# Optimization experiments

Measured on AMD Instinct MI355X. Metric: run time of the kernel, lower is better.

## Reference

```python
import jax, jax.numpy as jnp
import numpy as np

R = 8            # LoRA rank (cfg.EXPERT_LOW_RANK)
E = 4            # expert count for proj (cfg.EXPERT_NUM)
TOPK_PCT = 50    # cfg.topk_tempalte == cfg.topk_search == 50, percent mode


def linear_experts(x, W, b, routeW, A, Bm, scaling):
    # LinearExperts.forward: frozen linear + softmax-routed sum of LoRA experts.
    res = x @ W.T + b
    rw = jax.nn.softmax((x @ routeW.T).astype(jnp.float32), axis=-1).astype(res.dtype)  # [B,N,E]
    z = jnp.einsum('bnc,erc->bner', x, A)      # [B,N,E,r]
    d = jnp.einsum('bner,ecr->bnec', z, Bm)    # [B,N,E,C_out]
    return res + jnp.einsum('bne,bnec->bnc', rw, d) * scaling


def merged_qkv(x, W, b, A, Bm, scaling):
    # loralib MergedLinear, enable_lora=[True,True,True]: grouped LoRA over q/k/v blocks.
    base = x @ W.T + b                          # [B,N,3C]
    z = jnp.einsum('bnc,grc->bngr', x, A)       # [B,N,3,r]
    d = jnp.einsum('bngr,gcr->bngc', z, Bm)     # [B,N,3,C]
    Bsz, N = x.shape[0], x.shape[1]
    return base + d.reshape(Bsz, N, -1) * scaling


def softmax_w_top(attn, top):
    # topk -> exp(v - v_max) -> normalize -> scatter back into zeros (rest exactly 0)
    vals, idx = jax.lax.top_k(attn, top)        # vals sorted desc, vals[...,0] is max
    ex = jnp.exp(vals - vals[..., :1])
    ex = ex / jnp.sum(ex, axis=-1, keepdims=True)
    Bh, Hh, Mh, _ = attn.shape
    bi = jnp.arange(Bh)[:, None, None, None]
    hi = jnp.arange(Hh)[None, :, None, None]
    mi = jnp.arange(Mh)[None, None, :, None]
    return jnp.zeros_like(attn).at[bi, hi, mi, idx].set(ex.astype(attn.dtype))


def setup_inputs() -> dict:
    key = jax.random.key(0)
    ks = jax.random.split(key, 32)
    B, N_m, N_s, C, H = 2, 576, 1024, 768, 12
    N = N_m + N_s
    hd = C // H
    N_mem = 1600
    s = 0.02
    inp = {
        'x': jax.random.normal(ks[0], (B, N, C), jnp.float32),
        'id_total': jax.random.normal(ks[1], (B, N_m, C), jnp.float32),
        'mem_k': jax.random.normal(ks[2], (B, H, N_mem, hd), jnp.float32),
        'mem_v': jax.random.normal(ks[3], (B, H, N_mem, hd), jnp.float32),
        # qkv MergedLinear
        'W_qkv': jax.random.normal(ks[4], (3 * C, C), jnp.float32) * s,
        'b_qkv': jnp.zeros((3 * C,), jnp.float32),
        'A_qkv': jax.random.normal(ks[5], (3, R, C), jnp.float32) * s,
        'B_qkv': jax.random.normal(ks[6], (3, C, R), jnp.float32) * s,
        # proj LinearExperts (lora_num=E)
        'W_proj': jax.random.normal(ks[7], (C, C), jnp.float32) * s,
        'b_proj': jnp.zeros((C,), jnp.float32),
        'routeW_proj': jax.random.normal(ks[8], (E, C), jnp.float32) * s,
        'A_proj': jax.random.normal(ks[9], (E, R, C), jnp.float32) * s,
        'B_proj': jax.random.normal(ks[10], (E, C, R), jnp.float32) * s,
        # linear_ID_K LinearExperts (lora_num=1, out=num_heads)
        'W_idk': jax.random.normal(ks[11], (H, C), jnp.float32) * s,
        'b_idk': jnp.zeros((H,), jnp.float32),
        'routeW_idk': jax.random.normal(ks[12], (1, C), jnp.float32) * s,
        'A_idk': jax.random.normal(ks[13], (1, R, C), jnp.float32) * s,
        'B_idk': jax.random.normal(ks[14], (1, H, R), jnp.float32) * s,
        # linear_ID_V LinearExperts (lora_num=1, out=dim)
        'W_idv': jax.random.normal(ks[15], (C, C), jnp.float32) * s,
        'b_idv': jnp.zeros((C,), jnp.float32),
        'routeW_idv': jax.random.normal(ks[16], (1, C), jnp.float32) * s,
        'A_idv': jax.random.normal(ks[17], (1, R, C), jnp.float32) * s,
        'B_idv': jax.random.normal(ks[18], (1, C, R), jnp.float32) * s,
        'id_add': 1,
    }
    return inp


def reference(x, id_total, mem_k, mem_v,
              W_qkv, b_qkv, A_qkv, B_qkv,
              W_proj, b_proj, routeW_proj, A_proj, B_proj,
              W_idk, b_idk, routeW_idk, A_idk, B_idk,
              W_idv, b_idv, routeW_idv, A_idv, B_idv,
              id_add):
    B, N, C = x.shape
    H = 12
    hd = C // H
    N_m = id_total.shape[1]
    N_s = N - N_m
    scale = hd ** -0.5
    scaling = 1.0 / R  # lora_alpha=1 default

    qkv = merged_qkv(x, W_qkv, b_qkv, A_qkv, B_qkv, scaling)          # [B,N,3C]
    qkv = qkv.reshape(B, N, 3, H, hd).transpose(2, 0, 3, 1, 4)        # [3,B,H,N,hd]
    q, k, v = qkv[0], qkv[1], qkv[2]
    k_m, k_s = k[:, :, :N_m], k[:, :, N_m:]
    v_m, v_s = v[:, :, :N_m], v[:, :, N_m:]

    # key_value_id: ID gating fused into memory K/V (id_add=True path)
    ID_K = linear_experts(id_total, W_idk, b_idk, routeW_idk, A_idk, B_idk, scaling)  # [B,N_m,H]
    ID_V = linear_experts(id_total, W_idv, b_idv, routeW_idv, A_idv, B_idv, scaling)  # [B,N_m,C]
    k_m = k_m * (1.0 + jnp.tanh(ID_K)).transpose(0, 2, 1)[..., None]                  # [B,H,N_m,hd]
    v_m_flat = v_m.transpose(0, 2, 1, 3).reshape(B, N_m, C) + ID_V                    # [B,N_m,C]
    v_m = v_m_flat.reshape(B, N_m, H, hd).transpose(0, 2, 1, 3)                       # [B,H,N_m,hd]
    v_add_id = jnp.concatenate([v_m, v_s], axis=2)                                    # [B,H,N,hd]

    q = q * scale
    q_m, q_s = q[:, :, :N_m], q[:, :, N_m:]

    # memory-token attention with top-k softmax (percent mode)
    attn_m = jnp.einsum('bhmd,bhnd->bhmn', q_m, k_m)
    top_m = TOPK_PCT * N_m // 100
    attn_m = softmax_w_top(attn_m, top_m)
    x_m = jnp.einsum('bhmn,bhnd->bhmd', attn_m, v_m).transpose(0, 2, 1, 3).reshape(B, N_m, C)

    # search-token attention over [cached memory, all current tokens]
    k_full = jnp.concatenate([mem_k, k], axis=2)
    v_full = jnp.concatenate([mem_v, v_add_id], axis=2)
    L = k_full.shape[2]
    attn_s = jnp.einsum('bhsd,bhld->bhsl', q_s, k_full)
    top_s = TOPK_PCT * L // 100
    attn_s = softmax_w_top(attn_s, top_s)
    x_s = jnp.einsum('bhsl,bhld->bhsd', attn_s, v_full).transpose(0, 2, 1, 3).reshape(B, N_s, C)

    out = jnp.concatenate([x_m, x_s], axis=1)
    out = linear_experts(out, W_proj, b_proj, routeW_proj, A_proj, B_proj, scaling)
    return (out, k_m, v_m)
```

## Files before the change

kernel.cpp:

```cpp
#include <hip/hip_runtime.h>
#include <hip/hip_bf16.h>

#define BN 2
#define NH 12
#define NTOK 1600
#define NM 576
#define NS 1024
#define CD 768
#define HD 64

typedef unsigned short u16;
typedef unsigned int u32;
typedef __attribute__((ext_vector_type(8))) short short8;
typedef __attribute__((ext_vector_type(4))) float f32x4;

__device__ __forceinline__ float fbits(u32 u) { return __uint_as_float(u); }
__device__ __forceinline__ u16 f2b(float f) {
    u32 u = __float_as_uint(f);
    u32 r = u + 0x7FFFu + ((u >> 16) & 1u);
    return (u16)(r >> 16);
}
__device__ __forceinline__ float b2f(u16 s) { return fbits(((u32)s) << 16); }
__device__ __forceinline__ u32 flip16(u32 u) {
    return (u & 0x8000u) ? (0xFFFFu & ~u) : (u | 0x8000u);
}
__device__ __forceinline__ float key2f(u32 k) {
    u32 b = (k & 0x8000u) ? (k & 0x7FFFu) : (0xFFFFu & ~k);
    return fbits(b << 16);
}
__device__ __forceinline__ float wave_red(float p) {
#pragma unroll
    for (int off = 1; off < 64; off <<= 1) p += __shfl_xor(p, off);
    return p;
}

__device__ __forceinline__ float dot768_ff(const float* __restrict__ a,
                                           const float* __restrict__ b) {
    float s = 0.f;
    for (int c = 0; c < CD; c += 4) {
        float4 fa = *(const float4*)(a + c);
        float4 fb = *(const float4*)(b + c);
        s += fa.x * fb.x + fa.y * fb.y + fa.z * fb.z + fa.w * fb.w;
    }
    return s;
}

__global__ __launch_bounds__(256) void small_dots(const float* __restrict__ x,
                                                  const float* __restrict__ Aq,
                                                  float* __restrict__ zq,
                                                  const float* __restrict__ id,
                                                  const float* __restrict__ Aik,
                                                  const float* __restrict__ Aiv,
                                                  const float* __restrict__ Wik,
                                                  const float* __restrict__ bik,
                                                  const float* __restrict__ Bik,
                                                  float* __restrict__ ziv,
                                                  float* __restrict__ IDK) {
    __shared__ float dres[28];
    const int blk = blockIdx.x;
    const int tid = threadIdx.x, lane = tid & 63, wv = tid >> 6;
    if (blk < 3200) {
        const float* xr = x + (size_t)blk * CD;
#pragma unroll
        for (int t = 0; t < 6; ++t) {
            const int q = wv * 6 + t;
            const float* ar = Aq + (size_t)q * CD;
            float p = 0.f;
#pragma unroll
            for (int c = 0; c < 12; ++c) p += xr[lane + c * 64] * ar[lane + c * 64];
            p = wave_red(p);
            if (lane == 0) zq[(size_t)blk * 24 + q] = p;
        }
    } else {
        const int m = blk - 3200;
        const float* xr = id + (size_t)m * CD;
#pragma unroll
        for (int t = 0; t < 7; ++t) {
            const int q = wv * 7 + t;
            const float* ar = (q < 8) ? Aik + (size_t)q * CD
                            : (q < 16) ? Aiv + (size_t)(q - 8) * CD
                                       : Wik + (size_t)(q - 16) * CD;
            float p = 0.f;
#pragma unroll
            for (int c = 0; c < 12; ++c) p += xr[lane + c * 64] * ar[lane + c * 64];
            p = wave_red(p);
            if (lane == 0) dres[q] = p;
        }
        __syncthreads();
        if (tid < 8) ziv[(size_t)m * 8 + tid] = dres[8 + tid];
        if (tid < 12) {
            float v = dres[16 + tid] + bik[tid];
            float lo = 0.f;
#pragma unroll
            for (int r = 0; r < 8; ++r) lo += dres[r] * Bik[tid * 8 + r];
            IDK[m * NH + tid] = v + 0.125f * lo;
        }
    }
}

__global__ __launch_bounds__(256) void stage_all(const float* __restrict__ x,
                                                 const float* __restrict__ zq,
                                                 u16* __restrict__ x_aug,
                                                 const float* __restrict__ Wq,
                                                 const float* __restrict__ Bq,
                                                 u16* __restrict__ wqkv_aug,
                                                 const float* __restrict__ Wp,
                                                 const float* __restrict__ Bp,
                                                 u16* __restrict__ wproj_aug,
                                                 const float* __restrict__ mk,
                                                 u16* __restrict__ kseq,
                                                 const float* __restrict__ mv,
                                                 u16* __restrict__ vt,
                                                 const float* __restrict__ id,
                                                 const float* __restrict__ ziv,
                                                 u16* __restrict__ id_aug,
                                                 const float* __restrict__ Widv,
                                                 const float* __restrict__ Bidv,
                                                 u16* __restrict__ widv_aug) {
    __shared__ float tile[64][65];
    const int blk = blockIdx.x;
    const int tid = threadIdx.x;
    if (blk < 1250) {
        const int idx = blk * 256 + tid;
        const int m = idx / 100, c8 = idx - m * 100;
        short8 v;
        if (c8 < 96) {
            const float* s = x + (size_t)m * CD + c8 * 8;
#pragma unroll
            for (int i = 0; i < 8; ++i) v[i] = (short)f2b(s[i]);
        } else if (c8 < 99) {
            const float* s = zq + (size_t)m * 24 + (c8 - 96) * 8;
#pragma unroll
            for (int i = 0; i < 8; ++i) v[i] = (short)f2b(s[i]);
        } else {
#pragma unroll
            for (int i = 0; i < 8; ++i) v[i] = 0;
        }
        *(short8*)(x_aug + (size_t)m * 800 + c8 * 8) = v;
    } else if (blk < 2150) {
        const int idx = (blk - 1250) * 256 + tid;
        const int j = idx / 100, c8 = idx - j * 100;
        short8 v;
        if (c8 < 96) {
            const float* s = Wq + (size_t)j * CD + c8 * 8;
#pragma unroll
            for (int i = 0; i < 8; ++i) v[i] = (short)f2b(s[i]);
        } else if (c8 < 99) {
            const int g = j / CD, c = j - g * CD;
            const int gp = c8 - 96;
#pragma unroll
            for (int i = 0; i < 8; ++i)
                v[i] = (gp == g) ? (short)f2b(0.125f * Bq[((size_t)g * CD + c) * 8 + i])
                                 : (short)0;
        } else {
#pragma unroll
            for (int i = 0; i < 8; ++i) v[i] = 0;
        }
        *(short8*)(wqkv_aug + (size_t)j * 800 + c8 * 8) = v;
    } else if (blk < 2450) {
        const int idx = (blk - 2150) * 256 + tid;
        const int j = idx / 100, c8 = idx - j * 100;
        short8 v;
        if (c8 < 96) {
            const float* s = Wp + (size_t)j * CD + c8 * 8;
#pragma unroll
            for (int i = 0; i < 8; ++i) v[i] = (short)f2b(s[i]);
        } else {
            const int e = c8 - 96;
#pragma unroll
            for (int i = 0; i < 8; ++i) v[i] = (short)f2b(Bp[((size_t)e * CD + j) * 8 + i]);
        }
        *(short8*)(wproj_aug + (size_t)j * 800 + c8 * 8) = v;
    } else if (blk < 3650) {
        const int t = (blk - 2450) * 256 + tid;
        const size_t e = (size_t)t * 8;
        const size_t bh = e / (1600 * 64);
        const size_t rem = e - bh * (1600 * 64);
        const float4 f0 = *(const float4*)(mk + e);
        const float4 f1 = *(const float4*)(mk + e + 4);
        short8 s;
        s[0] = (short)f2b(f0.x); s[1] = (short)f2b(f0.y);
        s[2] = (short)f2b(f0.z); s[3] = (short)f2b(f0.w);
        s[4] = (short)f2b(f1.x); s[5] = (short)f2b(f1.y);
        s[6] = (short)f2b(f1.z); s[7] = (short)f2b(f1.w);
        *(short8*)(kseq + bh * (3200 * 64) + rem) = s;
    } else if (blk < 4250) {
        const int i = blk - 3650;
        const int kt = i % 25, bh = i / 25;
        const int r = tid >> 2, c0 = (tid & 3) * 16;
        const float* src = mv + ((size_t)bh * 1600 + (size_t)kt * 64 + r) * 64 + c0;
#pragma unroll
        for (int q = 0; q < 4; ++q) {
            const float4 f = *(const float4*)(src + q * 4);
            tile[r][c0 + q * 4 + 0] = f.x;
            tile[r][c0 + q * 4 + 1] = f.y;
            tile[r][c0 + q * 4 + 2] = f.z;
            tile[r][c0 + q * 4 + 3] = f.w;
        }
        __syncthreads();
        short8 s0, s1;
#pragma unroll
        for (int q = 0; q < 8; ++q) s0[q] = (short)f2b(tile[c0 + q][r]);
#pragma unroll
        for (int q = 0; q < 8; ++q) s1[q] = (short)f2b(tile[c0 + 8 + q][r]);
        u16* dst = vt + ((size_t)bh * 64 + r) * 3200 + (size_t)kt * 64 + c0;
        *(short8*)dst = s0;
        *(short8*)(dst + 8) = s1;
    } else if (blk < 4700) {
        const int idx = (blk - 4250) * 256 + tid;
        const int m = idx / 100, c8 = idx - m * 100;
        short8 v;
        if (c8 < 96) {
            const float* s = id + (size_t)m * CD + c8 * 8;
#pragma unroll
            for (int i = 0; i < 8; ++i) v[i] = (short)f2b(s[i]);
        } else if (c8 == 96) {
            const float* s = ziv + (size_t)m * 8;
#pragma unroll
            for (int i = 0; i < 8; ++i) v[i] = (short)f2b(s[i]);
        } else {
#pragma unroll
            for (int i = 0; i < 8; ++i) v[i] = 0;
        }
        *(short8*)(id_aug + (size_t)m * 800 + c8 * 8) = v;
    } else {
        const int idx = (blk - 4700) * 256 + tid;
        const int j = idx / 100, c8 = idx - j * 100;
        short8 v;
        if (c8 < 96) {
            const float* s = Widv + (size_t)j * CD + c8 * 8;
#pragma unroll
            for (int i = 0; i < 8; ++i) v[i] = (short)f2b(s[i]);
        } else if (c8 == 96) {
#pragma unroll
            for (int i = 0; i < 8; ++i) v[i] = (short)f2b(0.125f * Bidv[(size_t)j * 8 + i]);
        } else {
#pragma unroll
            for (int i = 0; i < 8; ++i) v[i] = 0;
        }
        *(short8*)(widv_aug + (size_t)j * 800 + c8 * 8) = v;
    }
}

template <int MODE>
__global__ __launch_bounds__(MODE == 0 ? 256 : 128) void
gemm16_kernel(const u16* __restrict__ A16, const u16* __restrict__ B16,
              const float* __restrict__ bias, const float* __restrict__ IDK,
              u16* __restrict__ qbh, u16* __restrict__ kseq, u16* __restrict__ vt,
              float* __restrict__ okm, float* __restrict__ ovm,
              float* __restrict__ io) {
    const int tid = threadIdx.x;
    const int lane = tid & 63, wv = tid >> 6;
    const int quad = lane >> 4, n16 = lane & 15;
    int m0, n0;
    if (MODE == 0) {
        m0 = blockIdx.y * 128 + (wv >> 1) * 64;
        n0 = blockIdx.x * 128 + (wv & 1) * 64;
    } else {
        m0 = blockIdx.y * 64;
        n0 = blockIdx.x * 128 + wv * 64;
    }

    f32x4 acc[4][4];
#pragma unroll
    for (int a = 0; a < 4; ++a)
#pragma unroll
        for (int b = 0; b < 4; ++b) acc[a][b] = (f32x4){0.f, 0.f, 0.f, 0.f};

    const u16* ap = A16 + (size_t)(m0 + n16) * 800 + quad * 8;
    const u16* bp = B16 + (size_t)(n0 + n16) * 800 + quad * 8;
#pragma unroll 2
    for (int k0 = 0; k0 < 800; k0 += 32) {
        short8 aA[4], aB[4];
#pragma unroll
        for (int c = 0; c < 4; ++c) {
            aA[c] = *(const short8*)(ap + (size_t)c * 16 * 800 + k0);
            aB[c] = *(const short8*)(bp + (size_t)c * 16 * 800 + k0);
        }
#pragma unroll
        for (int mc = 0; mc < 4; ++mc)
#pragma unroll
            for (int nc = 0; nc < 4; ++nc)
                acc[mc][nc] =
                    __builtin_amdgcn_mfma_f32_16x16x32_bf16(aA[mc], aB[nc], acc[mc][nc], 0, 0, 0);
    }

    if (MODE == 0) {
        const int g = n0 / CD;
        const int hq = (n0 % CD) >> 6;
#pragma unroll
        for (int mc = 0; mc < 4; ++mc) {
#pragma unroll
            for (int r = 0; r < 4; ++r) {
                const int m = m0 + mc * 16 + quad * 4 + r;
                const int b = m / NTOK, n = m - (m / NTOK) * NTOK;
                const size_t bh = (size_t)(b * NH + hq);
                float gate = 0.f;
                if (g == 1 && n < NM) gate = 1.f + tanhf(IDK[(b * NM + n) * NH + hq]);
#pragma unroll
                for (int nc = 0; nc < 4; ++nc) {
                    const int d = nc * 16 + n16;
                    const int j = n0 + d;
                    const float val = acc[mc][nc][r] + bias[j];
                    const size_t om = (bh * NM + n) * 64 + d;
                    if (g == 0) {
                        qbh[(bh * NTOK + n) * 64 + d] = f2b(val * 0.125f);
                    } else if (g == 1) {
                        kseq[(bh * 3200 + 1600 + n) * 64 + d] = f2b(val);
                        if (n < NM) okm[om] = val * gate;
                    } else {
                        float vv = val;
                        if (n < NM) {
                            vv = val + ovm[om];
                            ovm[om] = vv;
                        }
                        vt[(bh * 64 + d) * 3200 + 1600 + n] = f2b(vv);
                    }
                }
            }
        }
    } else if (MODE == 1) {
#pragma unroll
        for (int mc = 0; mc < 4; ++mc) {
#pragma unroll
            for (int r = 0; r < 4; ++r) {
                const int m = m0 + mc * 16 + quad * 4 + r;
#pragma unroll
                for (int nc = 0; nc < 4; ++nc) {
                    const int j = n0 + nc * 16 + n16;
                    io[(size_t)m * CD + j] = acc[mc][nc][r] + bias[j];
                }
            }
        }
    } else {
#pragma unroll
        for (int mc = 0; mc < 4; ++mc) {
#pragma unroll
            for (int r = 0; r < 4; ++r) {
                const int m = m0 + mc * 16 + quad * 4 + r;
                const int b = m / NM, n = m - (m / NM) * NM;
#pragma unroll
                for (int nc = 0; nc < 4; ++nc) {
                    const int j = n0 + nc * 16 + n16;
                    const int h = j >> 6, d = j & 63;
                    ovm[(((size_t)(b * NH + h)) * NM + n) * 64 + d] = acc[mc][nc][r] + bias[j];
                }
            }
        }
    }
}

template <int L, bool KF32>
__global__ __launch_bounds__(512) void attn10_kernel(const u16* __restrict__ qbh,
                                                     const u16* __restrict__ Kb,
                                                     const float* __restrict__ Kf,
                                                     const u16* __restrict__ vt,
                                                     float* __restrict__ aob,
                                                     int top, int row_start, int krows,
                                                     int vtoff) {
    constexpr int LP = L + 8;
    constexpr int NCHT = L / 16;
    constexpr int NCH = (NCHT + 7) / 8;
    constexpr bool FULL = (NCHT % 8) == 0;
    constexpr int PAIRS = L / 2;
    constexpr int NPIT = (PAIRS + 63) / 64;
    constexpr bool PFULL = (PAIRS % 64) == 0;
    extern __shared__ __align__(16) u16 smem[];
    u16* wgt = smem;
    u32* hist = (u32*)(smem + 16 * LP);
    float* obuf = (float*)hist;
    float* rowmax = (float*)(hist + 8192);
    float* invtot = rowmax + 128;
    float* Mrow = invtot + 16;
    u32* selb = (u32*)(Mrow + 16);
    u32* Trow = selb + 16;
    u32* wantr = Trow + 16;

    const int tid = threadIdx.x;
    const int lane = tid & 63, wv = tid >> 6;
    const int quad = lane >> 4, n16 = lane & 15;
    const int rep = (n16 & 1) * 4096;
    const int bh = blockIdx.y;
    const int bb = bh / NH, hh = bh - bb * NH;
    const int r0 = row_start + blockIdx.x * 16;

    for (int i = tid; i < 8192; i += 512) hist[i] = 0;

    short8 aQ0, aQ1;
    {
        const u16* qp = qbh + ((size_t)bh * NTOK + r0 + n16) * 64;
        aQ0 = *(const short8*)(qp + quad * 8);
        aQ1 = *(const short8*)(qp + 32 + quad * 8);
    }
    __syncthreads();

    float rmax[4] = {-3.4e38f, -3.4e38f, -3.4e38f, -3.4e38f};
#pragma unroll
    for (int i = 0; i < NCH; ++i) {
        const int c = wv + i * 8;
        if (FULL || c < NCHT) {
            const int l0 = c << 4;
            short8 fb0, fb1;
            if (KF32) {
                const float* kp = Kf + ((size_t)bh * krows + l0 + n16) * 64 + quad * 8;
                const float4 x0 = *(const float4*)kp;
                const float4 x1 = *(const float4*)(kp + 4);
                const float4 y0 = *(const float4*)(kp + 32);
                const float4 y1 = *(const float4*)(kp + 36);
                fb0[0] = (short)f2b(x0.x); fb0[1] = (short)f2b(x0.y);
                fb0[2] = (short)f2b(x0.z); fb0[3] = (short)f2b(x0.w);
                fb0[4] = (short)f2b(x1.x); fb0[5] = (short)f2b(x1.y);
                fb0[6] = (short)f2b(x1.z); fb0[7] = (short)f2b(x1.w);
                fb1[0] = (short)f2b(y0.x); fb1[1] = (short)f2b(y0.y);
                fb1[2] = (short)f2b(y0.z); fb1[3] = (short)f2b(y0.w);
                fb1[4] = (short)f2b(y1.x); fb1[5] = (short)f2b(y1.y);
                fb1[6] = (short)f2b(y1.z); fb1[7] = (short)f2b(y1.w);
            } else {
                const u16* kp = Kb + ((size_t)bh * krows + l0 + n16) * 64 + quad * 8;
                fb0 = *(const short8*)kp;
                fb1 = *(const short8*)(kp + 32);
            }
            f32x4 d = {0.f, 0.f, 0.f, 0.f};
            d = __builtin_amdgcn_mfma_f32_16x16x32_bf16(aQ0, fb0, d, 0, 0, 0);
            d = __builtin_amdgcn_mfma_f32_16x16x32_bf16(aQ1, fb1, d, 0, 0, 0);
            const u16 w0 = f2b(d[0]), w1 = f2b(d[1]), w2 = f2b(d[2]), w3 = f2b(d[3]);
#pragma unroll
            for (int r = 0; r < 4; ++r) rmax[r] = fmaxf(rmax[r], d[r]);
            wgt[(size_t)(quad * 4 + 0) * LP + l0 + n16] = w0;
            wgt[(size_t)(quad * 4 + 1) * LP + l0 + n16] = w1;
            wgt[(size_t)(quad * 4 + 2) * LP + l0 + n16] = w2;
            wgt[(size_t)(quad * 4 + 3) * LP + l0 + n16] = w3;
            atomicAdd(&hist[rep + (quad * 4 + 0) * 256 + (flip16((u32)w0) >> 8)], 1u);
            atomicAdd(&hist[rep + (quad * 4 + 1) * 256 + (flip16((u32)w1) >> 8)], 1u);
            atomicAdd(&hist[rep + (quad * 4 + 2) * 256 + (flip16((u32)w2) >> 8)], 1u);
            atomicAdd(&hist[rep + (quad * 4 + 3) * 256 + (flip16((u32)w3) >> 8)], 1u);
        }
    }
#pragma unroll
    for (int off = 1; off < 16; off <<= 1) {
#pragma unroll
        for (int r = 0; r < 4; ++r) rmax[r] = fmaxf(rmax[r], __shfl_xor(rmax[r], off));
    }
    if (n16 == 0) {
#pragma unroll
        for (int r = 0; r < 4; ++r) rowmax[wv * 16 + quad * 4 + r] = rmax[r];
    }
    __syncthreads();

#pragma unroll
    for (int rp = 0; rp < 2; ++rp) {
        const int rr = wv + 8 * rp;
        float M = -3.4e38f;
#pragma unroll
        for (int w = 0; w < 8; ++w) M = fmaxf(M, rowmax[w * 16 + rr]);
        if (lane == 0) Mrow[rr] = M;
        u32 hh4[4];
#pragma unroll
        for (int j = 0; j < 4; ++j)
            hh4[j] = hist[rr * 256 + 4 * lane + j] + hist[4096 + rr * 256 + 4 * lane + j];
        const u32 s = hh4[0] + hh4[1] + hh4[2] + hh4[3];
        u32 sum = s;
#pragma unroll
        for (int off = 1; off < 64; off <<= 1) {
            const u32 t = __shfl_down(sum, off);
            if (lane + off < 64) sum += t;
        }
        int cnt = (int)(sum - s);
        const int want = top;
        for (int j = 3; j >= 0; --j) {
            const int c = (int)hh4[j];
            if (cnt < want && cnt + c >= want) {
                selb[rr] = (u32)(4 * lane + j);
                wantr[rr] = (u32)(want - cnt);
            }
            cnt += c;
        }
    }
    __syncthreads();
    for (int i = tid; i < 8192; i += 512) hist[i] = 0;
    __syncthreads();

#pragma unroll
    for (int rp = 0; rp < 2; ++rp) {
        const int rr = wv + 8 * rp;
        const u32* row32 = (const u32*)(wgt + (size_t)rr * LP);
        const u32 sel1 = selb[rr];
        const float M = Mrow[rr];
#pragma unroll
        for (int i = 0; i < NPIT; ++i) {
            if (PFULL || lane + 64 * i < PAIRS) {
                const u32 pr = row32[lane + 64 * i];
                const u32 k0 = flip16(pr & 0xffffu), k1 = flip16(pr >> 16);
                if ((k0 >> 8) == sel1) atomicAdd(&hist[rep + rr * 256 + (k0 & 255u)], 1u);
                if ((k1 >> 8) == sel1) atomicAdd(&hist[rep + rr * 256 + (k1 & 255u)], 1u);
            }
        }
        __threadfence_block();
        {
            u32 hh4[4];
#pragma unroll
            for (int j = 0; j < 4; ++j)
                hh4[j] = hist[rr * 256 + 4 * lane + j] + hist[4096 + rr * 256 + 4 * lane + j];
            const u32 s = hh4[0] + hh4[1] + hh4[2] + hh4[3];
            u32 sum = s;
#pragma unroll
            for (int off = 1; off < 64; off <<= 1) {
                const u32 t = __shfl_down(sum, off);
                if (lane + off < 64) sum += t;
            }
            int cnt = (int)(sum - s);
            const int want = (int)wantr[rr];
            for (int j = 3; j >= 0; --j) {
                const int c = (int)hh4[j];
                if (cnt < want && cnt + c >= want) {
                    const u32 T = (sel1 << 8) | (u32)(4 * lane + j);
                    Trow[rr] = T;
                    invtot[rr] = (float)(want - cnt) * __expf(fminf(key2f(T) - M, 0.f));
                }
                cnt += c;
            }
        }
        __threadfence_block();
        {
            const u32 T = Trow[rr];
            u32* roww = (u32*)(wgt + (size_t)rr * LP);
            float ps = 0.f;
#pragma unroll
            for (int i = 0; i < NPIT; ++i) {
                if (PFULL || lane + 64 * i < PAIRS) {
                    const u32 pr = roww[lane + 64 * i];
                    const u32 k0 = flip16(pr & 0xffffu), k1 = flip16(pr >> 16);
                    float e0 = 0.f, e1 = 0.f;
                    if (k0 >= T) {
                        e0 = __expf(fminf(b2f((u16)(pr & 0xffffu)) - M, 0.f));
                        if (k0 > T) ps += e0;
                    }
                    if (k1 >= T) {
                        e1 = __expf(fminf(b2f((u16)(pr >> 16)) - M, 0.f));
                        if (k1 > T) ps += e1;
                    }
                    roww[lane + 64 * i] = (u32)f2b(e0) | ((u32)f2b(e1) << 16);
                }
            }
            ps = wave_red(ps);
            if (lane == 0) invtot[rr] = 1.f / fmaxf(invtot[rr] + ps, 1e-30f);
        }
    }
    __syncthreads();

    {
        const int half = wv & 1, dc = wv >> 1;
        constexpr int PVI = (L / 2) / 32;
        const int kbeg = half * (L / 2);
        const u16* vp =
            vt + ((size_t)bh * 64 + dc * 16 + n16) * 3200 + vtoff + quad * 8 + kbeg;
        const u16* wrow2 = wgt + (size_t)n16 * LP + quad * 8 + kbeg;
        f32x4 acc = {0.f, 0.f, 0.f, 0.f};
#pragma unroll 8
        for (int i = 0; i < PVI; ++i) {
            const short8 a = *(const short8*)(wrow2 + i * 32);
            const short8 bf = *(const short8*)(vp + i * 32);
            acc = __builtin_amdgcn_mfma_f32_16x16x32_bf16(a, bf, acc, 0, 0, 0);
        }
#pragma unroll
        for (int r = 0; r < 4; ++r) {
            const int rowi = quad * 4 + r;
            obuf[(half * 16 + rowi) * 64 + dc * 16 + n16] = acc[r] * invtot[rowi];
        }
    }
    __syncthreads();
#pragma unroll
    for (int ii = 0; ii < 2; ++ii) {
        const int idx = tid + ii * 512;
        const int rowi = idx >> 6, dd = idx & 63;
        aob[((size_t)bb * NTOK + r0 + rowi) * CD + hh * 64 + dd] =
            obuf[rowi * 64 + dd] + obuf[(16 + rowi) * 64 + dd];
    }
}

__global__ __launch_bounds__(256) void coef_kernel(const float* __restrict__ aob,
                                                   const float* __restrict__ rW,
                                                   const float* __restrict__ Ap,
                                                   float* __restrict__ coef) {
    __shared__ float rl[8][4];
    __shared__ float rw[8][4];
    const int slot = threadIdx.x >> 5, lane = threadIdx.x & 31;
    const int m = blockIdx.x * 8 + slot;
    const float* xr = aob + (size_t)m * CD;
    const float z = dot768_ff(xr, Ap + (size_t)lane * CD);
    if (lane < 4) rl[slot][lane] = dot768_ff(xr, rW + (size_t)lane * CD);
    __syncthreads();
    if (lane == 0) {
        const float mx = fmaxf(fmaxf(rl[slot][0], rl[slot][1]), fmaxf(rl[slot][2], rl[slot][3]));
        const float e0 = __expf(rl[slot][0] - mx), e1 = __expf(rl[slot][1] - mx);
        const float e2 = __expf(rl[slot][2] - mx), e3 = __expf(rl[slot][3] - mx);
        const float is = 1.f / (e0 + e1 + e2 + e3);
        rw[slot][0] = e0 * is; rw[slot][1] = e1 * is; rw[slot][2] = e2 * is; rw[slot][3] = e3 * is;
    }
    __syncthreads();
    coef[(size_t)m * 32 + lane] = rw[slot][lane >> 3] * z * 0.125f;
}

__global__ __launch_bounds__(256) void cvt_aobaug(const float* __restrict__ aob,
                                                  const float* __restrict__ coef,
                                                  u16* __restrict__ dst) {
    const int idx = blockIdx.x * 256 + threadIdx.x;
    const int m = idx / 100, c8 = idx - m * 100;
    short8 v;
    if (c8 < 96) {
        const float* s = aob + (size_t)m * CD + c8 * 8;
#pragma unroll
        for (int i = 0; i < 8; ++i) v[i] = (short)f2b(s[i]);
    } else {
        const float* s = coef + (size_t)m * 32 + (c8 - 96) * 8;
#pragma unroll
        for (int i = 0; i < 8; ++i) v[i] = (short)f2b(s[i]);
    }
    *(short8*)(dst + (size_t)m * 800 + c8 * 8) = v;
}

extern "C" void kernel_launch(void* const* d_in, const int* in_sizes, int n_in,
                              void* d_out, int out_size, void* d_ws, size_t ws_size,
                              hipStream_t stream) {
    const float* x = (const float*)d_in[0];
    const float* id_total = (const float*)d_in[1];
    const float* mem_k = (const float*)d_in[2];
    const float* mem_v = (const float*)d_in[3];
    const float* W_qkv = (const float*)d_in[4];
    const float* b_qkv = (const float*)d_in[5];
    const float* A_qkv = (const float*)d_in[6];
    const float* B_qkv = (const float*)d_in[7];
    const float* W_proj = (const float*)d_in[8];
    const float* b_proj = (const float*)d_in[9];
    const float* routeW_proj = (const float*)d_in[10];
    const float* A_proj = (const float*)d_in[11];
    const float* B_proj = (const float*)d_in[12];
    const float* W_idk = (const float*)d_in[13];
    const float* b_idk = (const float*)d_in[14];
    const float* A_idk = (const float*)d_in[16];
    const float* B_idk = (const float*)d_in[17];
    const float* W_idv = (const float*)d_in[18];
    const float* b_idv = (const float*)d_in[19];
    const float* A_idv = (const float*)d_in[21];
    const float* B_idv = (const float*)d_in[22];

    float* io = (float*)d_out;
    float* o_km = io + (size_t)BN * NTOK * CD;
    float* o_vm = o_km + (size_t)BN * NH * NM * HD;

    u16* x_aug = (u16*)io;
    u16* wqkv_aug = x_aug + 2560000;
    u16* widv_aug = (u16*)o_km;

    u16* qbh = (u16*)d_ws;
    u16* kseq = qbh + 2457600;
    u16* vt = kseq + 4915200;
    float* zq = (float*)(vt + 4915200);
    float* ziv = zq + 76800;
    float* IDK = ziv + 9216;
    float* coef = IDK + 13824;
    u16* wproj_aug = (u16*)(coef + 102400);
    u16* id_aug = qbh;

    const int smem_seq = 16 * (3200 + 8) * 2 + 33600;
    const int smem_mem = 16 * (NM + 8) * 2 + 33600;
    hipFuncSetAttribute((const void*)attn10_kernel<3200, false>,
                        hipFuncAttributeMaxDynamicSharedMemorySize, smem_seq);
    hipFuncSetAttribute((const void*)attn10_kernel<NM, true>,
                        hipFuncAttributeMaxDynamicSharedMemorySize, smem_mem);

    small_dots<<<4352, 256, 0, stream>>>(x, A_qkv, zq, id_total, A_idk, A_idv,
                                         W_idk, b_idk, B_idk, ziv, IDK);
    stage_all<<<5000, 256, 0, stream>>>(x, zq, x_aug, W_qkv, B_qkv, wqkv_aug,
                                        W_proj, B_proj, wproj_aug, mem_k, kseq,
                                        mem_v, vt, id_total, ziv, id_aug,
                                        W_idv, B_idv, widv_aug);
    gemm16_kernel<2><<<dim3(6, 18), 128, 0, stream>>>(id_aug, widv_aug, b_idv, nullptr,
                                                      nullptr, nullptr, nullptr, nullptr,
                                                      o_vm, nullptr);
    gemm16_kernel<0><<<dim3(18, 25), 256, 0, stream>>>(x_aug, wqkv_aug, b_qkv, IDK,
                                                       qbh, kseq, vt, o_km, o_vm, nullptr);

    attn10_kernel<NM, true><<<dim3(NM / 16, BN * NH), 512, smem_mem, stream>>>(
        qbh, nullptr, o_km, vt, io, NM / 2, 0, NM, 1600);
    attn10_kernel<3200, false><<<dim3(NS / 16, BN * NH), 512, smem_seq, stream>>>(
        qbh, kseq, nullptr, vt, io, 1600, NM, 3200, 0);

    coef_kernel<<<400, 256, 0, stream>>>(io, routeW_proj, A_proj, coef);
    cvt_aobaug<<<1250, 256, 0, stream>>>(io, coef, kseq);
    gemm16_kernel<1><<<dim3(6, 50), 128, 0, stream>>>(kseq, wproj_aug, b_proj, nullptr,
                                                      nullptr, nullptr, nullptr, nullptr,
                                                      nullptr, io);
}
```

Before: 609.2 us.

## Merge both attention launches into one kernel and batch K/V loads

Merges the memory-token and search-token attention kernels into a single launch that branches on blockIdx.x, so the short memory blocks can run alongside the long search blocks instead of forming a separate tail. The QK loop now issues loads for groups of key chunks before their MFMAs, and the PV loop prefetches five V fragments ahead, to raise memory-level parallelism. It also sets launch bounds to two blocks per CU. The cost is higher register pressure, and the memory-path blocks now reserve the full shared-memory allocation sized for the long path.

```diff
diff --git a/kernel.cpp b/kernel.cpp
--- a/kernel.cpp
+++ b/kernel.cpp
@@ -351,13 +351,11 @@
 }
 
 template <int L, bool KF32>
-__global__ __launch_bounds__(512) void attn10_kernel(const u16* __restrict__ qbh,
-                                                     const u16* __restrict__ Kb,
-                                                     const float* __restrict__ Kf,
-                                                     const u16* __restrict__ vt,
-                                                     float* __restrict__ aob,
-                                                     int top, int row_start, int krows,
-                                                     int vtoff) {
+__device__ void attn_body(u16* smem,
+                          const u16* __restrict__ qbh, const u16* __restrict__ Kb,
+                          const float* __restrict__ Kf, const u16* __restrict__ vt,
+                          float* __restrict__ aob, int top, int row_start, int krows,
+                          int vtoff, int blkx, int bh) {
     constexpr int LP = L + 8;
     constexpr int NCHT = L / 16;
     constexpr int NCH = (NCHT + 7) / 8;
@@ -365,7 +363,7 @@
     constexpr int PAIRS = L / 2;
     constexpr int NPIT = (PAIRS + 63) / 64;
     constexpr bool PFULL = (PAIRS % 64) == 0;
-    extern __shared__ __align__(16) u16 smem[];
+    constexpr int GRP = KF32 ? 2 : 5;
     u16* wgt = smem;
     u32* hist = (u32*)(smem + 16 * LP);
     float* obuf = (float*)hist;
@@ -380,9 +378,8 @@
     const int lane = tid & 63, wv = tid >> 6;
     const int quad = lane >> 4, n16 = lane & 15;
     const int rep = (n16 & 1) * 4096;
-    const int bh = blockIdx.y;
     const int bb = bh / NH, hh = bh - bb * NH;
-    const int r0 = row_start + blockIdx.x * 16;
+    const int r0 = row_start + blkx * 16;
 
     for (int i = tid; i < 8192; i += 512) hist[i] = 0;
 
@@ -396,44 +393,58 @@
 
     float rmax[4] = {-3.4e38f, -3.4e38f, -3.4e38f, -3.4e38f};
 #pragma unroll
-    for (int i = 0; i < NCH; ++i) {
-        const int c = wv + i * 8;
-        if (FULL || c < NCHT) {
-            const int l0 = c << 4;
-            short8 fb0, fb1;
-            if (KF32) {
-                const float* kp = Kf + ((size_t)bh * krows + l0 + n16) * 64 + quad * 8;
-                const float4 x0 = *(const float4*)kp;
-                const float4 x1 = *(const float4*)(kp + 4);
-                const float4 y0 = *(const float4*)(kp + 32);
-                const float4 y1 = *(const float4*)(kp + 36);
-                fb0[0] = (short)f2b(x0.x); fb0[1] = (short)f2b(x0.y);
-                fb0[2] = (short)f2b(x0.z); fb0[3] = (short)f2b(x0.w);
-                fb0[4] = (short)f2b(x1.x); fb0[5] = (short)f2b(x1.y);
-                fb0[6] = (short)f2b(x1.z); fb0[7] = (short)f2b(x1.w);
-                fb1[0] = (short)f2b(y0.x); fb1[1] = (short)f2b(y0.y);
-                fb1[2] = (short)f2b(y0.z); fb1[3] = (short)f2b(y0.w);
-                fb1[4] = (short)f2b(y1.x); fb1[5] = (short)f2b(y1.y);
-                fb1[6] = (short)f2b(y1.z); fb1[7] = (short)f2b(y1.w);
-            } else {
-                const u16* kp = Kb + ((size_t)bh * krows + l0 + n16) * 64 + quad * 8;
-                fb0 = *(const short8*)kp;
-                fb1 = *(const short8*)(kp + 32);
-            }
-            f32x4 d = {0.f, 0.f, 0.f, 0.f};
-            d = __builtin_amdgcn_mfma_f32_16x16x32_bf16(aQ0, fb0, d, 0, 0, 0);
-            d = __builtin_amdgcn_mfma_f32_16x16x32_bf16(aQ1, fb1, d, 0, 0, 0);
-            const u16 w0 = f2b(d[0]), w1 = f2b(d[1]), w2 = f2b(d[2]), w3 = f2b(d[3]);
-#pragma unroll
-            for (int r = 0; r < 4; ++r) rmax[r] = fmaxf(rmax[r], d[r]);
-            wgt[(size_t)(quad * 4 + 0) * LP + l0 + n16] = w0;
-            wgt[(size_t)(quad * 4 + 1) * LP + l0 + n16] = w1;
-            wgt[(size_t)(quad * 4 + 2) * LP + l0 + n16] = w2;
-            wgt[(size_t)(quad * 4 + 3) * LP + l0 + n16] = w3;
-            atomicAdd(&hist[rep + (quad * 4 + 0) * 256 + (flip16((u32)w0) >> 8)], 1u);
-            atomicAdd(&hist[rep + (quad * 4 + 1) * 256 + (flip16((u32)w1) >> 8)], 1u);
-            atomicAdd(&hist[rep + (quad * 4 + 2) * 256 + (flip16((u32)w2) >> 8)], 1u);
-            atomicAdd(&hist[rep + (quad * 4 + 3) * 256 + (flip16((u32)w3) >> 8)], 1u);
+    for (int g = 0; g < NCH; g += GRP) {
+        short8 fb0[GRP], fb1[GRP];
+#pragma unroll
+        for (int i = 0; i < GRP; ++i) {
+            const int ci = g + i;
+            const int c = wv + ci * 8;
+            if (ci < NCH && (FULL || c < NCHT)) {
+                const int l0 = c << 4;
+                if (KF32) {
+                    const float* kp = Kf + ((size_t)bh * krows + l0 + n16) * 64 + quad * 8;
+                    const float4 x0 = *(const float4*)kp;
+                    const float4 x1 = *(const float4*)(kp + 4);
+                    const float4 y0 = *(const float4*)(kp + 32);
+                    const float4 y1 = *(const float4*)(kp + 36);
+                    short8 t0, t1;
+                    t0[0] = (short)f2b(x0.x); t0[1] = (short)f2b(x0.y);
+                    t0[2] = (short)f2b(x0.z); t0[3] = (short)f2b(x0.w);
+                    t0[4] = (short)f2b(x1.x); t0[5] = (short)f2b(x1.y);
+                    t0[6] = (short)f2b(x1.z); t0[7] = (short)f2b(x1.w);
+                    t1[0] = (short)f2b(y0.x); t1[1] = (short)f2b(y0.y);
+                    t1[2] = (short)f2b(y0.z); t1[3] = (short)f2b(y0.w);
+                    t1[4] = (short)f2b(y1.x); t1[5] = (short)f2b(y1.y);
+                    t1[6] = (short)f2b(y1.z); t1[7] = (short)f2b(y1.w);
+                    fb0[i] = t0; fb1[i] = t1;
+                } else {
+                    const u16* kp = Kb + ((size_t)bh * krows + l0 + n16) * 64 + quad * 8;
+                    fb0[i] = *(const short8*)kp;
+                    fb1[i] = *(const short8*)(kp + 32);
+                }
+            }
+        }
+#pragma unroll
+        for (int i = 0; i < GRP; ++i) {
+            const int ci = g + i;
+            const int c = wv + ci * 8;
+            if (ci < NCH && (FULL || c < NCHT)) {
+                const int l0 = c << 4;
+                f32x4 d = {0.f, 0.f, 0.f, 0.f};
+                d = __builtin_amdgcn_mfma_f32_16x16x32_bf16(aQ0, fb0[i], d, 0, 0, 0);
+                d = __builtin_amdgcn_mfma_f32_16x16x32_bf16(aQ1, fb1[i], d, 0, 0, 0);
+                const u16 w0 = f2b(d[0]), w1 = f2b(d[1]), w2 = f2b(d[2]), w3 = f2b(d[3]);
+#pragma unroll
+                for (int r = 0; r < 4; ++r) rmax[r] = fmaxf(rmax[r], d[r]);
+                wgt[(size_t)(quad * 4 + 0) * LP + l0 + n16] = w0;
+                wgt[(size_t)(quad * 4 + 1) * LP + l0 + n16] = w1;
+                wgt[(size_t)(quad * 4 + 2) * LP + l0 + n16] = w2;
+                wgt[(size_t)(quad * 4 + 3) * LP + l0 + n16] = w3;
+                atomicAdd(&hist[rep + (quad * 4 + 0) * 256 + (flip16((u32)w0) >> 8)], 1u);
+                atomicAdd(&hist[rep + (quad * 4 + 1) * 256 + (flip16((u32)w1) >> 8)], 1u);
+                atomicAdd(&hist[rep + (quad * 4 + 2) * 256 + (flip16((u32)w2) >> 8)], 1u);
+                atomicAdd(&hist[rep + (quad * 4 + 3) * 256 + (flip16((u32)w3) >> 8)], 1u);
+            }
         }
     }
 #pragma unroll
@@ -551,16 +562,25 @@
     {
         const int half = wv & 1, dc = wv >> 1;
         constexpr int PVI = (L / 2) / 32;
+        constexpr int GP = 5;
         const int kbeg = half * (L / 2);
         const u16* vp =
             vt + ((size_t)bh * 64 + dc * 16 + n16) * 3200 + vtoff + quad * 8 + kbeg;
         const u16* wrow2 = wgt + (size_t)n16 * LP + quad * 8 + kbeg;
         f32x4 acc = {0.f, 0.f, 0.f, 0.f};
-#pragma unroll 8
-        for (int i = 0; i < PVI; ++i) {
-            const short8 a = *(const short8*)(wrow2 + i * 32);
-            const short8 bf = *(const short8*)(vp + i * 32);
-            acc = __builtin_amdgcn_mfma_f32_16x16x32_bf16(a, bf, acc, 0, 0, 0);
+#pragma unroll
+        for (int gg = 0; gg < PVI; gg += GP) {
+            short8 bfr[GP];
+#pragma unroll
+            for (int i = 0; i < GP; ++i)
+                if (gg + i < PVI) bfr[i] = *(const short8*)(vp + (gg + i) * 32);
+#pragma unroll
+            for (int i = 0; i < GP; ++i) {
+                if (gg + i < PVI) {
+                    const short8 a = *(const short8*)(wrow2 + (gg + i) * 32);
+                    acc = __builtin_amdgcn_mfma_f32_16x16x32_bf16(a, bfr[i], acc, 0, 0, 0);
+                }
+            }
         }
 #pragma unroll
         for (int r = 0; r < 4; ++r) {
@@ -575,6 +595,21 @@
         const int rowi = idx >> 6, dd = idx & 63;
         aob[((size_t)bb * NTOK + r0 + rowi) * CD + hh * 64 + dd] =
             obuf[rowi * 64 + dd] + obuf[(16 + rowi) * 64 + dd];
+    }
+}
+
+__global__ __launch_bounds__(512, 2) void attn_merged(const u16* __restrict__ qbh,
+                                                      const u16* __restrict__ kseq,
+                                                      const float* __restrict__ okm,
+                                                      const u16* __restrict__ vt,
+                                                      float* __restrict__ aob) {
+    extern __shared__ __align__(16) u16 smem[];
+    if (blockIdx.x < NM / 16) {
+        attn_body<NM, true>(smem, qbh, nullptr, okm, vt, aob, NM / 2, 0, NM, 1600,
+                            blockIdx.x, blockIdx.y);
+    } else {
+        attn_body<3200, false>(smem, qbh, kseq, nullptr, vt, aob, 1600, NM, 3200, 0,
+                               blockIdx.x - NM / 16, blockIdx.y);
     }
 }
 
@@ -663,11 +698,8 @@
     u16* id_aug = qbh;
 
     const int smem_seq = 16 * (3200 + 8) * 2 + 33600;
-    const int smem_mem = 16 * (NM + 8) * 2 + 33600;
-    hipFuncSetAttribute((const void*)attn10_kernel<3200, false>,
+    hipFuncSetAttribute((const void*)attn_merged,
                         hipFuncAttributeMaxDynamicSharedMemorySize, smem_seq);
-    hipFuncSetAttribute((const void*)attn10_kernel<NM, true>,
-                        hipFuncAttributeMaxDynamicSharedMemorySize, smem_mem);
 
     small_dots<<<4352, 256, 0, stream>>>(x, A_qkv, zq, id_total, A_idk, A_idv,
                                          W_idk, b_idk, B_idk, ziv, IDK);
@@ -681,10 +713,8 @@
     gemm16_kernel<0><<<dim3(18, 25), 256, 0, stream>>>(x_aug, wqkv_aug, b_qkv, IDK,
                                                        qbh, kseq, vt, o_km, o_vm, nullptr);
 
-    attn10_kernel<NM, true><<<dim3(NM / 16, BN * NH), 512, smem_mem, stream>>>(
-        qbh, nullptr, o_km, vt, io, NM / 2, 0, NM, 1600);
-    attn10_kernel<3200, false><<<dim3(NS / 16, BN * NH), 512, smem_seq, stream>>>(
-        qbh, kseq, nullptr, vt, io, 1600, NM, 3200, 0);
+    attn_merged<<<dim3(NM / 16 + NS / 16, BN * NH), 512, smem_seq, stream>>>(
+        qbh, kseq, o_km, vt, io);
 
     coef_kernel<<<400, 256, 0, stream>>>(io, routeW_proj, A_proj, coef);
     cvt_aobaug<<<1250, 256, 0, stream>>>(io, coef, kseq);
```

Result: slower. 649.1 us (+6.6%).
